# Performance work log

Hardware: AMD Instinct MI355X
Metric: run time of the kernel (lower is better)

The kernel has to match this reference:

```python
import jax, jax.numpy as jnp
import numpy as np
from jax import lax

DN = ('NCHW', 'OIHW', 'NCHW')

def _edge_bank():
    # All eight fixed stencils embedded in 5x5 (3x3 kernels zero-padded to center),
    # equivalent to the original per-kernel SAME conv. Order matches torch.cat order:
    # sobel_x, sobel_y, diag1, diag2, laplacian, gradient5x5, scharr_x, scharr_y
    k3 = [
        [[-1, 0, 1], [-2, 0, 2], [-1, 0, 1]],            # sobel_x
        [[-1, -2, -1], [0, 0, 0], [1, 2, 1]],            # sobel_y
        [[0, 1, 2], [-1, 0, 1], [-2, -1, 0]],            # diag1
        [[-2, -1, 0], [-1, 0, 1], [0, 1, 2]],            # diag2
        [[0, 1, 0], [1, -4, 1], [0, 1, 0]],              # laplacian
    ]
    g5 = [[-1, -2, 0, 2, 1], [-2, -3, 0, 3, 2], [-3, -4, 0, 4, 3],
          [-2, -3, 0, 3, 2], [-1, -2, 0, 2, 1]]          # gradient5x5
    s3 = [
        [[-3, 0, 3], [-10, 0, 10], [-3, 0, 3]],          # scharr_x
        [[-3, -10, -3], [0, 0, 0], [3, 10, 3]],          # scharr_y
    ]
    ks = []
    for k in k3:
        ks.append(np.pad(np.asarray(k, np.float32), 1))
    ks.append(np.asarray(g5, np.float32))
    for k in s3:
        ks.append(np.pad(np.asarray(k, np.float32), 1))
    return jnp.asarray(np.stack(ks)[:, None, :, :])  # [8,1,5,5]

EDGE_BANK = _edge_bank()

def _conv(x, w, p):
    return lax.conv_general_dilated(x, w, (1, 1), [(p, p), (p, p)], dimension_numbers=DN)

def setup_inputs() -> dict:
    key = jax.random.key(0)
    k = jax.random.split(key, 7)
    x  = jax.random.normal(k[0], (8, 1, 512, 512), jnp.float32)
    w1 = jax.random.normal(k[1], (32, 9, 3, 3), jnp.float32) * 0.05
    b1 = jax.random.normal(k[2], (32,), jnp.float32) * 0.01
    w2 = jax.random.normal(k[3], (16, 32, 3, 3), jnp.float32) * 0.05
    b2 = jax.random.normal(k[4], (16,), jnp.float32) * 0.01
    wr = jax.random.normal(k[5], (16, 1, 1, 1), jnp.float32) * 0.05
    br = jax.random.normal(k[6], (16,), jnp.float32) * 0.01
    return {"x": x, "w1": w1, "b1": b1, "w2": w2, "b2": b2, "wr": wr, "br": br}

def reference(x, w1, b1, w2, b2, wr, br):
    grads = _conv(x, EDGE_BANK, 2)                         # [B,8,H,W] all stencils in one pass
    feats = jnp.concatenate([grads, x], axis=1)            # [B,9,H,W]
    h = jax.nn.relu(_conv(feats, w1, 1) + b1[None, :, None, None])
    fused = jax.nn.relu(_conv(h, w2, 1) + b2[None, :, None, None])
    residual = _conv(x, wr, 0) + br[None, :, None, None]
    return fused + residual
```

## Files before the change

### kernel.cpp

```cpp
#include <hip/hip_runtime.h>
#include <hip/hip_bf16.h>


typedef __attribute__((ext_vector_type(8))) short bf16x8;
typedef __attribute__((ext_vector_type(4))) float f32x4;

#define XS_S 28

#define WS_A2   5120
#define WS_SB   9728
#define WS_FLT  5120
#define WS_WEFF 12800
#define WS_BYTES 30720

__device__ const float EB[9][5][5] = {
 {{0,0,0,0,0},{0,-1,0,1,0},{0,-2,0,2,0},{0,-1,0,1,0},{0,0,0,0,0}},
 {{0,0,0,0,0},{0,-1,-2,-1,0},{0,0,0,0,0},{0,1,2,1,0},{0,0,0,0,0}},
 {{0,0,0,0,0},{0,0,1,2,0},{0,-1,0,1,0},{0,-2,-1,0,0},{0,0,0,0,0}},
 {{0,0,0,0,0},{0,-2,-1,0,0},{0,-1,0,1,0},{0,0,1,2,0},{0,0,0,0,0}},
 {{0,0,0,0,0},{0,0,1,0,0},{0,1,-4,1,0},{0,0,1,0,0},{0,0,0,0,0}},
 {{-1,-2,0,2,1},{-2,-3,0,3,2},{-3,-4,0,4,3},{-2,-3,0,3,2},{-1,-2,0,2,1}},
 {{0,0,0,0,0},{0,-3,0,3,0},{0,-10,0,10,0},{0,-3,0,3,0},{0,0,0,0,0}},
 {{0,0,0,0,0},{0,-3,-10,-3,0},{0,0,0,0,0},{0,3,10,3,0},{0,0,0,0,0}},
 {{0,0,0,0,0},{0,0,0,0,0},{0,0,1,0,0},{0,0,0,0,0},{0,0,0,0,0}},
};

__device__ __forceinline__ unsigned short f2bf(float f) {
    union { float f; unsigned u; } v; v.f = f;
    unsigned u = v.u + 0x7fffu + ((v.u >> 16) & 1u);
    return (unsigned short)(u >> 16);
}

__device__ __forceinline__ float weff_tap(const float* __restrict__ w1,
                                          int oc, int dy, int dx) {
    float s = 0.f;
    for (int ch = 0; ch < 9; ++ch)
        for (int ty = 0; ty < 3; ++ty)
            for (int tx = 0; tx < 3; ++tx) {
                int sy = dy - ty, sx = dx - tx;
                if (sy >= 0 && sy < 5 && sx >= 0 && sx < 5)
                    s += w1[(oc * 9 + ch) * 9 + ty * 3 + tx] * EB[ch][sy][sx];
            }
    return s;
}

__global__ __launch_bounds__(256) void setup_frags(
    const float* __restrict__ w1, const float* __restrict__ b1,
    const float* __restrict__ w2, const float* __restrict__ b2,
    const float* __restrict__ wr, const float* __restrict__ br,
    short* __restrict__ ws)
{
    __shared__ float w1s[2592];
    __shared__ float w2s[4608];
    __shared__ float ebs[225];
    const int tid = threadIdx.x;

    for (int i = tid; i < 2592; i += 256) w1s[i] = w1[i];
    for (int i = tid; i < 4608; i += 256) w2s[i] = w2[i];
    if (tid < 225) ebs[tid] = ((const float*)EB)[tid];
    __syncthreads();

    for (int idx = tid; idx < 5120; idx += 256) {
        int i = idx & 7, lane = (idx >> 3) & 63, rest = idx >> 9;
        int mt = rest / 5, ks = rest - 5 * mt;
        int n = lane & 15, lg = lane >> 4;
        int k = 32 * ks + 8 * lg + i;
        int g = k >> 4, ch = k & 15;
        float w = (g < 9 && ch < 9) ? w1s[(mt * 16 + n) * 81 + ch * 9 + g] : 0.f;
        ws[idx] = (short)f2bf(w);
    }
    for (int idx = tid; idx < 4608; idx += 256) {
        int i = idx & 7, lane = (idx >> 3) & 63, ks = idx >> 9;
        int n = lane & 15, lg = lane >> 4;
        int ic = 8 * lg + i;
        ws[WS_A2 + idx] = (short)f2bf(w2s[n * 288 + ic * 9 + ks]);
    }
    for (int idx = tid; idx < 512; idx += 256) {
        int i = idx & 7, lane = idx >> 3;
        int n = lane & 15, lg = lane >> 4;
        int k = 8 * lg + i;
        float v = (k < 25 && n < 9) ? ebs[n * 25 + k] : 0.f;
        ws[WS_SB + idx] = (short)f2bf(v);
    }
    for (int idx = tid; idx < 2048; idx += 256) {
        int i = idx & 7, lane = (idx >> 3) & 63, rest = idx >> 9;
        int mt = rest >> 1, ks = rest & 1;
        int n = lane & 15, lg = lane >> 4;
        int dy = 4 * ks + lg, dx = i;
        float s = 0.f;
        if (dy < 7 && dx < 7) {
            int oc = mt * 16 + n;
            for (int ch = 0; ch < 9; ++ch)
                for (int ty = 0; ty < 3; ++ty) {
                    int sy = dy - ty;
                    if (sy < 0 || sy >= 5) continue;
                    for (int tx = 0; tx < 3; ++tx) {
                        int sx = dx - tx;
                        if (sx >= 0 && sx < 5)
                            s += w1s[(oc * 9 + ch) * 9 + ty * 3 + tx] * ebs[ch * 25 + sy * 5 + sx];
                    }
                }
        }
        ws[WS_WEFF + idx] = (short)f2bf(s);
    }
    if (tid < 64) {
        int lg = tid >> 4;
        float* wf = (float*)ws + WS_FLT + tid * 20;
        for (int r = 0; r < 4; ++r) {
            wf[r]      = b1[lg * 4 + r];
            wf[4 + r]  = b1[16 + lg * 4 + r];
            wf[8 + r]  = b2[lg * 4 + r];
            wf[12 + r] = wr[lg * 4 + r];
            wf[16 + r] = br[lg * 4 + r];
        }
    }
}

template<bool USE_WS>
__global__ __launch_bounds__(256, 3) void edge_interior2(
    const float* __restrict__ x,  const float* __restrict__ w1, const float* __restrict__ b1,
    const float* __restrict__ w2, const float* __restrict__ b2,
    const float* __restrict__ wr, const float* __restrict__ br,
    const short* __restrict__ ws, float* __restrict__ out)
{
    __shared__ long long pool[39936 / 8];
    __shared__ short xs[24 * 40 + 8];
    short* hs    = (short*)pool;
    float* stage = (float*)pool;

    const int tid  = threadIdx.x;
    const int lane = tid & 63;
    const int wave = tid >> 6;
    const int n    = lane & 15;
    const int lg   = lane >> 4;
    const int bx = blockIdx.x * 32, by = blockIdx.y * 16, b = blockIdx.z;

    for (int i = tid; i < 480; i += 256) {
        int r = i / 20, c2 = i % 20;
        int gy = by - 4 + r;  gy = gy < 0 ? 0 : (gy > 511 ? 511 : gy);
        int gx = bx - 4 + 2 * c2; gx = gx < 0 ? 0 : (gx > 510 ? 510 : gx);
        const float2 v = *reinterpret_cast<const float2*>(&x[((size_t)b * 512 + gy) * 512 + gx]);
        __hip_bfloat162 p0 = __float22bfloat162_rn(make_float2(v.x, v.y));
        *reinterpret_cast<unsigned*>(&xs[r * 40 + 2 * c2]) = *reinterpret_cast<unsigned*>(&p0);
    }

    bf16x8 wa[2][2], a2[9];
    float b1v[2][4], b2v[4], wrv[4], brv[4];
    if (USE_WS) {
#pragma unroll
        for (int mt = 0; mt < 2; ++mt)
#pragma unroll
            for (int ks = 0; ks < 2; ++ks)
                wa[mt][ks] = *reinterpret_cast<const bf16x8*>(
                    &ws[WS_WEFF + ((mt * 2 + ks) * 64 + lane) * 8]);
#pragma unroll
        for (int ks = 0; ks < 9; ++ks)
            a2[ks] = *reinterpret_cast<const bf16x8*>(&ws[WS_A2 + (ks * 64 + lane) * 8]);
        const float* wf = (const float*)ws + WS_FLT + lane * 20;
        f32x4 t0 = *reinterpret_cast<const f32x4*>(wf);
        f32x4 t1 = *reinterpret_cast<const f32x4*>(wf + 4);
        f32x4 t2 = *reinterpret_cast<const f32x4*>(wf + 8);
        f32x4 t3 = *reinterpret_cast<const f32x4*>(wf + 12);
        f32x4 t4 = *reinterpret_cast<const f32x4*>(wf + 16);
#pragma unroll
        for (int r = 0; r < 4; ++r) {
            b1v[0][r] = t0[r]; b1v[1][r] = t1[r];
            b2v[r] = t2[r]; wrv[r] = t3[r]; brv[r] = t4[r];
        }
    } else {
#pragma unroll
        for (int mt = 0; mt < 2; ++mt)
#pragma unroll
            for (int ks = 0; ks < 2; ++ks)
#pragma unroll
                for (int i = 0; i < 8; ++i) {
                    int dy = 4 * ks + lg, dx = i;
                    float s = (dy < 7 && dx < 7) ? weff_tap(w1, mt * 16 + n, dy, dx) : 0.f;
                    wa[mt][ks][i] = (short)f2bf(s);
                }
#pragma unroll
        for (int ks = 0; ks < 9; ++ks)
#pragma unroll
            for (int i = 0; i < 8; ++i)
                a2[ks][i] = (short)f2bf(w2[n * 288 + (8 * lg + i) * 9 + ks]);
#pragma unroll
        for (int r = 0; r < 4; ++r) {
            b1v[0][r] = b1[lg * 4 + r]; b1v[1][r] = b1[16 + lg * 4 + r];
            b2v[r] = b2[lg * 4 + r]; wrv[r] = wr[lg * 4 + r]; brv[r] = br[lg * 4 + r];
        }
    }

    __syncthreads();

    for (int t = wave; t < 39; t += 4) {
        int p  = t * 16 + n;
        int pc = p < 611 ? p : 611;
        int r1 = pc / 34, c1 = pc - 34 * r1;
        int base = r1 * 40 + c1;
        f32x4 acc0 = {0.f,0.f,0.f,0.f}, acc1 = {0.f,0.f,0.f,0.f};
#pragma unroll
        for (int ks = 0; ks < 2; ++ks) {
            const int dy = 4 * ks + lg;
            bf16x8 bv = {0,0,0,0,0,0,0,0};
            if (dy < 7) {
                const short* rp = &xs[base + dy * 40];
#pragma unroll
                for (int i = 0; i < 8; ++i) bv[i] = rp[i];
            }
            acc0 = __builtin_amdgcn_mfma_f32_16x16x32_bf16(wa[0][ks], bv, acc0, 0, 0, 0);
            acc1 = __builtin_amdgcn_mfma_f32_16x16x32_bf16(wa[1][ks], bv, acc1, 0, 0, 0);
        }
        if (p < 612) {
            __hip_bfloat162 q0 = __float22bfloat162_rn(make_float2(
                fmaxf(acc0[0] + b1v[0][0], 0.f), fmaxf(acc0[1] + b1v[0][1], 0.f)));
            __hip_bfloat162 q1 = __float22bfloat162_rn(make_float2(
                fmaxf(acc0[2] + b1v[0][2], 0.f), fmaxf(acc0[3] + b1v[0][3], 0.f)));
            uint2 W0; W0.x = *reinterpret_cast<unsigned*>(&q0);
            W0.y = *reinterpret_cast<unsigned*>(&q1);
            *reinterpret_cast<uint2*>(&hs[(((lg >> 1)) * 624 + p) * 8 + 4 * (lg & 1)]) = W0;
            __hip_bfloat162 q2 = __float22bfloat162_rn(make_float2(
                fmaxf(acc1[0] + b1v[1][0], 0.f), fmaxf(acc1[1] + b1v[1][1], 0.f)));
            __hip_bfloat162 q3 = __float22bfloat162_rn(make_float2(
                fmaxf(acc1[2] + b1v[1][2], 0.f), fmaxf(acc1[3] + b1v[1][3], 0.f)));
            uint2 W1; W1.x = *reinterpret_cast<unsigned*>(&q2);
            W1.y = *reinterpret_cast<unsigned*>(&q3);
            *reinterpret_cast<uint2*>(&hs[((2 + (lg >> 1)) * 624 + p) * 8 + 4 * (lg & 1)]) = W1;
        }
    }
    __syncthreads();

    const int hbase = lg * 624 * 8;
    f32x4 oreg[8];
#pragma unroll
    for (int j = 0; j < 8; ++j) {
        const int tj = wave + 4 * j;
        const int oy = tj >> 1, hh = tj & 1;
        f32x4 acc = {0.f,0.f,0.f,0.f};
#pragma unroll
        for (int ks = 0; ks < 9; ++ks) {
            const int dy = ks / 3, dx = ks - 3 * (ks / 3);
            const int px = (oy + dy) * 34 + 16 * hh + n + dx;
            bf16x8 hf = *reinterpret_cast<const bf16x8*>(&hs[hbase + px * 8]);
            acc = __builtin_amdgcn_mfma_f32_16x16x32_bf16(a2[ks], hf, acc, 0, 0, 0);
        }
        __hip_bfloat16 xh = *reinterpret_cast<const __hip_bfloat16*>(
            &xs[(oy + 4) * 40 + 16 * hh + n + 4]);
        float xv = __bfloat162float(xh);
        f32x4 o;
#pragma unroll
        for (int r = 0; r < 4; ++r)
            o[r] = fmaxf(acc[r] + b2v[r], 0.f) + wrv[r] * xv + brv[r];
        oreg[j] = o;
    }
    __syncthreads();

#pragma unroll
    for (int j = 0; j < 8; ++j) {
        const int tj = wave + 4 * j;
        const int oy = tj >> 1, hh = tj & 1;
#pragma unroll
        for (int r = 0; r < 4; ++r)
            stage[(lg * 4 + r) * 576 + oy * 36 + 16 * hh + n] = oreg[j][r];
    }
    __syncthreads();

#pragma unroll
    for (int k = 0; k < 8; ++k) {
        int idx = k * 256 + tid;
        int c   = idx & 7;
        int row = (idx >> 3) & 15;
        int oc  = idx >> 7;
        f32x4 v = *reinterpret_cast<const f32x4*>(&stage[oc * 576 + row * 36 + 4 * c]);
        __builtin_nontemporal_store(v, reinterpret_cast<f32x4*>(
            &out[(((size_t)b * 16 + oc) * 512 + (by + row)) * 512 + bx + 4 * c]));
    }
}

template<bool USE_WS>
__global__ __launch_bounds__(256, 4) void edge_border(
    const float* __restrict__ x,  const float* __restrict__ w1, const float* __restrict__ b1,
    const float* __restrict__ w2, const float* __restrict__ b2,
    const float* __restrict__ wr, const float* __restrict__ br,
    const short* __restrict__ ws, float* __restrict__ out)
{
    __shared__ short fs2[2 * 400 * 8];
    __shared__ short hs4[4 * 324 * 8];
    __shared__ short xs[24 * XS_S];

    const int tid  = threadIdx.x;
    const int lane = tid & 63;
    const int wave = tid >> 6;
    const int n    = lane & 15;
    const int lg   = lane >> 4;

    int idx = blockIdx.x, tx, ty;
    if      (idx < 32) { tx = idx;      ty = 0;  }
    else if (idx < 64) { tx = idx - 32; ty = 31; }
    else if (idx < 94) { tx = 0;        ty = idx - 63; }
    else               { tx = 31;       ty = idx - 93; }
    const int bx = tx * 16, by = ty * 16, b = blockIdx.z;

    for (int i = tid; i < 576; i += 256) {
        int r = i / 24, c = i % 24;
        int gy = by - 4 + r, gx = bx - 4 + c;
        float v = 0.f;
        if (gy >= 0 && gy < 512 && gx >= 0 && gx < 512) v = x[((size_t)b * 512 + gy) * 512 + gx];
        __hip_bfloat16 h = __float2bfloat16(v);
        xs[r * XS_S + c] = *reinterpret_cast<short*>(&h);
    }

    bf16x8 a1[2][5], a2[9], sb;
    float b1v[2][4], b2v[4], wrv[4], brv[4];
    if (USE_WS) {
#pragma unroll
        for (int mt = 0; mt < 2; ++mt)
#pragma unroll
            for (int ks = 0; ks < 5; ++ks)
                a1[mt][ks] = *reinterpret_cast<const bf16x8*>(&ws[((mt * 5 + ks) * 64 + lane) * 8]);
#pragma unroll
        for (int ks = 0; ks < 9; ++ks)
            a2[ks] = *reinterpret_cast<const bf16x8*>(&ws[WS_A2 + (ks * 64 + lane) * 8]);
        sb = *reinterpret_cast<const bf16x8*>(&ws[WS_SB + lane * 8]);
        const float* wf = (const float*)ws + WS_FLT + lane * 20;
        f32x4 t0 = *reinterpret_cast<const f32x4*>(wf);
        f32x4 t1 = *reinterpret_cast<const f32x4*>(wf + 4);
        f32x4 t2 = *reinterpret_cast<const f32x4*>(wf + 8);
        f32x4 t3 = *reinterpret_cast<const f32x4*>(wf + 12);
        f32x4 t4 = *reinterpret_cast<const f32x4*>(wf + 16);
#pragma unroll
        for (int r = 0; r < 4; ++r) {
            b1v[0][r] = t0[r]; b1v[1][r] = t1[r];
            b2v[r] = t2[r]; wrv[r] = t3[r]; brv[r] = t4[r];
        }
    } else {
#pragma unroll
        for (int mt = 0; mt < 2; ++mt)
#pragma unroll
            for (int ks = 0; ks < 5; ++ks)
#pragma unroll
                for (int i = 0; i < 8; ++i) {
                    int k = 32 * ks + 8 * lg + i;
                    int g = k >> 4, ch = k & 15;
                    float w = (g < 9 && ch < 9) ? w1[(mt * 16 + n) * 81 + ch * 9 + g] : 0.f;
                    a1[mt][ks][i] = (short)f2bf(w);
                }
#pragma unroll
        for (int ks = 0; ks < 9; ++ks)
#pragma unroll
            for (int i = 0; i < 8; ++i)
                a2[ks][i] = (short)f2bf(w2[n * 288 + (8 * lg + i) * 9 + ks]);
#pragma unroll
        for (int i = 0; i < 8; ++i) {
            int k = 8 * lg + i;
            float v = (k < 25 && n < 9) ? EB[n][k / 5][k % 5] : 0.f;
            sb[i] = (short)f2bf(v);
        }
#pragma unroll
        for (int r = 0; r < 4; ++r) {
            b1v[0][r] = b1[lg * 4 + r]; b1v[1][r] = b1[16 + lg * 4 + r];
            b2v[r] = b2[lg * 4 + r]; wrv[r] = wr[lg * 4 + r]; brv[r] = br[lg * 4 + r];
        }
    }

    int toff[8];
#pragma unroll
    for (int i = 0; i < 8; ++i) {
        int k = 8 * lg + i;
        int t = k < 25 ? k : 24;
        toff[i] = (t / 5) * XS_S + (t % 5);
    }
    int boff[5];
#pragma unroll
    for (int ks = 0; ks < 5; ++ks) {
        int g = 2 * ks + (lg >> 1); if (g > 8) g = 8;
        int dy = g / 3, dx = g - 3 * dy;
        boff[ks] = (lg & 1) * 3200 + (dy * 20 + dx) * 8;
    }

    __syncthreads();

    for (int t = wave; t < 25; t += 4) {
        int px = t * 16 + n;
        int r = px / 20, c = px - 20 * r;
        const short* base = &xs[r * XS_S + c];
        bf16x8 bv;
#pragma unroll
        for (int i = 0; i < 8; ++i) bv[i] = base[toff[i]];
        f32x4 f = {0.f, 0.f, 0.f, 0.f};
        f = __builtin_amdgcn_mfma_f32_16x16x32_bf16(sb, bv, f, 0, 0, 0);
        int fy = by + r - 2, fx = bx + c - 2;
        float m = (fy >= 0 && fy < 512 && fx >= 0 && fx < 512) ? 1.f : 0.f;
        __hip_bfloat162 p0 = __float22bfloat162_rn(make_float2(f[0] * m, f[1] * m));
        __hip_bfloat162 p1 = __float22bfloat162_rn(make_float2(f[2] * m, f[3] * m));
        uint2 wv;
        wv.x = *reinterpret_cast<unsigned*>(&p0);
        wv.y = *reinterpret_cast<unsigned*>(&p1);
        *reinterpret_cast<uint2*>(&fs2[((lg >> 1) * 400 + px) * 8 + 4 * (lg & 1)]) = wv;
    }
    __syncthreads();

    for (int t = wave; t < 21; t += 4) {
        int p  = t * 16 + n;
        int pc = p < 323 ? p : 323;
        int r1 = pc / 18, c1 = pc - 18 * r1;
        int base = (r1 * 20 + c1) * 8;
        f32x4 acc0 = {0.f,0.f,0.f,0.f}, acc1 = {0.f,0.f,0.f,0.f};
#pragma unroll
        for (int ks = 0; ks < 5; ++ks) {
            bf16x8 bf = *reinterpret_cast<const bf16x8*>(&fs2[base + boff[ks]]);
            acc0 = __builtin_amdgcn_mfma_f32_16x16x32_bf16(a1[0][ks], bf, acc0, 0, 0, 0);
            acc1 = __builtin_amdgcn_mfma_f32_16x16x32_bf16(a1[1][ks], bf, acc1, 0, 0, 0);
        }
        if (p < 324) {
            int hy = by - 1 + r1, hx = bx - 1 + c1;
            float m = (hy >= 0 && hy < 512 && hx >= 0 && hx < 512) ? 1.f : 0.f;
            __hip_bfloat162 q0 = __float22bfloat162_rn(make_float2(
                fmaxf(acc0[0] + b1v[0][0], 0.f) * m, fmaxf(acc0[1] + b1v[0][1], 0.f) * m));
            __hip_bfloat162 q1 = __float22bfloat162_rn(make_float2(
                fmaxf(acc0[2] + b1v[0][2], 0.f) * m, fmaxf(acc0[3] + b1v[0][3], 0.f) * m));
            uint2 W0; W0.x = *reinterpret_cast<unsigned*>(&q0);
            W0.y = *reinterpret_cast<unsigned*>(&q1);
            *reinterpret_cast<uint2*>(&hs4[((lg >> 1) * 324 + p) * 8 + 4 * (lg & 1)]) = W0;
            __hip_bfloat162 q2 = __float22bfloat162_rn(make_float2(
                fmaxf(acc1[0] + b1v[1][0], 0.f) * m, fmaxf(acc1[1] + b1v[1][1], 0.f) * m));
            __hip_bfloat162 q3 = __float22bfloat162_rn(make_float2(
                fmaxf(acc1[2] + b1v[1][2], 0.f) * m, fmaxf(acc1[3] + b1v[1][3], 0.f) * m));
            uint2 W1; W1.x = *reinterpret_cast<unsigned*>(&q2);
            W1.y = *reinterpret_cast<unsigned*>(&q3);
            *reinterpret_cast<uint2*>(&hs4[((2 + (lg >> 1)) * 324 + p) * 8 + 4 * (lg & 1)]) = W1;
        }
    }
    __syncthreads();

    const int hbase = lg * 324 * 8;
#pragma unroll
    for (int j = 0; j < 4; ++j) {
        int oy = wave + 4 * j;
        f32x4 acc = {0.f,0.f,0.f,0.f};
#pragma unroll
        for (int ks = 0; ks < 9; ++ks) {
            const int dy = ks / 3, dx = ks - 3 * (ks / 3);
            bf16x8 hf = *reinterpret_cast<const bf16x8*>(
                &hs4[hbase + ((oy + dy) * 18 + n + dx) * 8]);
            acc = __builtin_amdgcn_mfma_f32_16x16x32_bf16(a2[ks], hf, acc, 0, 0, 0);
        }
        __hip_bfloat16 xh = *reinterpret_cast<const __hip_bfloat16*>(&xs[(oy + 4) * XS_S + n + 4]);
        float xv = __bfloat162float(xh);
        float* op = out + (((size_t)(b * 16 + lg * 4) * 512 + (by + oy)) * 512) + bx + n;
#pragma unroll
        for (int r = 0; r < 4; ++r) {
            float o = fmaxf(acc[r] + b2v[r], 0.f) + wrv[r] * xv + brv[r];
            __builtin_nontemporal_store(o, op);
            op += 262144;
        }
    }
}

extern "C" void kernel_launch(void* const* d_in, const int* in_sizes, int n_in,
                              void* d_out, int out_size, void* d_ws, size_t ws_size,
                              hipStream_t stream) {
    const float* x  = (const float*)d_in[0];
    const float* w1 = (const float*)d_in[1];
    const float* b1 = (const float*)d_in[2];
    const float* w2 = (const float*)d_in[3];
    const float* b2 = (const float*)d_in[4];
    const float* wr = (const float*)d_in[5];
    const float* br = (const float*)d_in[6];
    float* out = (float*)d_out;
    short* ws = (short*)d_ws;

    dim3 block(256);
    dim3 gin(16, 32, 8);
    dim3 gbd(124, 1, 8);
    if (ws_size >= WS_BYTES) {
        hipLaunchKernelGGL(setup_frags, dim3(1), dim3(256), 0, stream,
                           w1, b1, w2, b2, wr, br, ws);
        hipLaunchKernelGGL(edge_interior2<true>, gin, block, 0, stream,
                           x, w1, b1, w2, b2, wr, br, ws, out);
        hipLaunchKernelGGL(edge_border<true>, gbd, block, 0, stream,
                           x, w1, b1, w2, b2, wr, br, ws, out);
    } else {
        hipLaunchKernelGGL(edge_interior2<false>, gin, block, 0, stream,
                           x, w1, b1, w2, b2, wr, br, ws, out);
        hipLaunchKernelGGL(edge_border<false>, gbd, block, 0, stream,
                           x, w1, b1, w2, b2, wr, br, ws, out);
    }
}
```

Before: 114.3 us.

## Restructure interior kernel: direct global x loads, interleaved swizzled h layout, row-reuse conv2

The interior kernel no longer stages x in shared memory. It reads x straight from global memory and converts it to bf16 in registers. The h tile is stored as interleaved 32-channel pixel rows with an XOR swizzle, and the w2 fragments are reordered to match that layout. Conv2 now loads each h row fragment once and reuses it across four output rows, which cuts LDS reads. The grid skips the top and bottom tile rows, occupancy is raised to 4 blocks, and border stores become plain stores. The trade-off is more redundant global loads and extra register pressure.

New measurement: 107.9 us. -5.6%, faster.

```diff
diff --git a/kernel.cpp b/kernel.cpp
--- a/kernel.cpp
+++ b/kernel.cpp
@@ -11,7 +11,8 @@
 #define WS_SB   9728
 #define WS_FLT  5120
 #define WS_WEFF 12800
-#define WS_BYTES 30720
+#define WS_A2I  14848
+#define WS_BYTES 38912
 
 __device__ const float EB[9][5][5] = {
  {{0,0,0,0,0},{0,-1,0,1,0},{0,-2,0,2,0},{0,-1,0,1,0},{0,0,0,0,0}},
@@ -30,6 +31,9 @@
     unsigned u = v.u + 0x7fffu + ((v.u >> 16) & 1u);
     return (unsigned short)(u >> 16);
 }
+__device__ __forceinline__ unsigned pk(float lo, float hi) {
+    return (unsigned)f2bf(lo) | ((unsigned)f2bf(hi) << 16);
+}
 
 __device__ __forceinline__ float weff_tap(const float* __restrict__ w1,
                                           int oc, int dy, int dx) {
@@ -74,6 +78,12 @@
         int n = lane & 15, lg = lane >> 4;
         int ic = 8 * lg + i;
         ws[WS_A2 + idx] = (short)f2bf(w2s[n * 288 + ic * 9 + ks]);
+    }
+    for (int idx = tid; idx < 4608; idx += 256) {
+        int i = idx & 7, lane = (idx >> 3) & 63, ks = idx >> 9;
+        int n = lane & 15, lg = lane >> 4;
+        int ic = ((i & 1) << 4) | (lg << 2) | ((i >> 1) & 3);
+        ws[WS_A2I + idx] = (short)f2bf(w2s[n * 288 + ic * 9 + ks]);
     }
     for (int idx = tid; idx < 512; idx += 256) {
         int i = idx & 7, lane = idx >> 3;
@@ -117,15 +127,14 @@
 }
 
 template<bool USE_WS>
-__global__ __launch_bounds__(256, 3) void edge_interior2(
+__global__ __launch_bounds__(256, 4) void edge_interior3(
     const float* __restrict__ x,  const float* __restrict__ w1, const float* __restrict__ b1,
     const float* __restrict__ w2, const float* __restrict__ b2,
     const float* __restrict__ wr, const float* __restrict__ br,
     const short* __restrict__ ws, float* __restrict__ out)
 {
-    __shared__ long long pool[39936 / 8];
-    __shared__ short xs[24 * 40 + 8];
-    short* hs    = (short*)pool;
+    __shared__ long long pool[39168 / 8];
+    short* hsS   = (short*)pool;
     float* stage = (float*)pool;
 
     const int tid  = threadIdx.x;
@@ -133,16 +142,10 @@
     const int wave = tid >> 6;
     const int n    = lane & 15;
     const int lg   = lane >> 4;
-    const int bx = blockIdx.x * 32, by = blockIdx.y * 16, b = blockIdx.z;
-
-    for (int i = tid; i < 480; i += 256) {
-        int r = i / 20, c2 = i % 20;
-        int gy = by - 4 + r;  gy = gy < 0 ? 0 : (gy > 511 ? 511 : gy);
-        int gx = bx - 4 + 2 * c2; gx = gx < 0 ? 0 : (gx > 510 ? 510 : gx);
-        const float2 v = *reinterpret_cast<const float2*>(&x[((size_t)b * 512 + gy) * 512 + gx]);
-        __hip_bfloat162 p0 = __float22bfloat162_rn(make_float2(v.x, v.y));
-        *reinterpret_cast<unsigned*>(&xs[r * 40 + 2 * c2]) = *reinterpret_cast<unsigned*>(&p0);
-    }
+    const int bx = blockIdx.x * 32;
+    const int by = (blockIdx.y + 1) * 16;
+    const int b  = blockIdx.z;
+    const float* xb = x + ((size_t)b << 18);
 
     bf16x8 wa[2][2], a2[9];
     float b1v[2][4], b2v[4], wrv[4], brv[4];
@@ -155,7 +158,7 @@
                     &ws[WS_WEFF + ((mt * 2 + ks) * 64 + lane) * 8]);
 #pragma unroll
         for (int ks = 0; ks < 9; ++ks)
-            a2[ks] = *reinterpret_cast<const bf16x8*>(&ws[WS_A2 + (ks * 64 + lane) * 8]);
+            a2[ks] = *reinterpret_cast<const bf16x8*>(&ws[WS_A2I + (ks * 64 + lane) * 8]);
         const float* wf = (const float*)ws + WS_FLT + lane * 20;
         f32x4 t0 = *reinterpret_cast<const f32x4*>(wf);
         f32x4 t1 = *reinterpret_cast<const f32x4*>(wf + 4);
@@ -181,86 +184,97 @@
 #pragma unroll
         for (int ks = 0; ks < 9; ++ks)
 #pragma unroll
-            for (int i = 0; i < 8; ++i)
-                a2[ks][i] = (short)f2bf(w2[n * 288 + (8 * lg + i) * 9 + ks]);
+            for (int i = 0; i < 8; ++i) {
+                int ic = ((i & 1) << 4) | (lg << 2) | ((i >> 1) & 3);
+                a2[ks][i] = (short)f2bf(w2[(n * 32 + ic) * 9 + ks]);
+            }
 #pragma unroll
         for (int r = 0; r < 4; ++r) {
             b1v[0][r] = b1[lg * 4 + r]; b1v[1][r] = b1[16 + lg * 4 + r];
             b2v[r] = b2[lg * 4 + r]; wrv[r] = wr[lg * 4 + r]; brv[r] = br[lg * 4 + r];
         }
     }
-
-    __syncthreads();
 
     for (int t = wave; t < 39; t += 4) {
         int p  = t * 16 + n;
         int pc = p < 611 ? p : 611;
         int r1 = pc / 34, c1 = pc - 34 * r1;
-        int base = r1 * 40 + c1;
+        int gxb = bx - 4 + c1; gxb = gxb < 0 ? 0 : (gxb > 504 ? 504 : gxb);
+        int gyb = by - 4 + r1;
         f32x4 acc0 = {0.f,0.f,0.f,0.f}, acc1 = {0.f,0.f,0.f,0.f};
 #pragma unroll
         for (int ks = 0; ks < 2; ++ks) {
             const int dy = 4 * ks + lg;
             bf16x8 bv = {0,0,0,0,0,0,0,0};
             if (dy < 7) {
-                const short* rp = &xs[base + dy * 40];
-#pragma unroll
-                for (int i = 0; i < 8; ++i) bv[i] = rp[i];
+                int gy = gyb + dy; gy = gy < 0 ? 0 : (gy > 511 ? 511 : gy);
+                const float* xp = xb + ((size_t)gy << 9) + gxb;
+                uint4 u;
+                u.x = pk(xp[0], xp[1]); u.y = pk(xp[2], xp[3]);
+                u.z = pk(xp[4], xp[5]); u.w = pk(xp[6], xp[7]);
+                bv = *reinterpret_cast<bf16x8*>(&u);
             }
             acc0 = __builtin_amdgcn_mfma_f32_16x16x32_bf16(wa[0][ks], bv, acc0, 0, 0, 0);
             acc1 = __builtin_amdgcn_mfma_f32_16x16x32_bf16(wa[1][ks], bv, acc1, 0, 0, 0);
         }
         if (p < 612) {
-            __hip_bfloat162 q0 = __float22bfloat162_rn(make_float2(
-                fmaxf(acc0[0] + b1v[0][0], 0.f), fmaxf(acc0[1] + b1v[0][1], 0.f)));
-            __hip_bfloat162 q1 = __float22bfloat162_rn(make_float2(
-                fmaxf(acc0[2] + b1v[0][2], 0.f), fmaxf(acc0[3] + b1v[0][3], 0.f)));
-            uint2 W0; W0.x = *reinterpret_cast<unsigned*>(&q0);
-            W0.y = *reinterpret_cast<unsigned*>(&q1);
-            *reinterpret_cast<uint2*>(&hs[(((lg >> 1)) * 624 + p) * 8 + 4 * (lg & 1)]) = W0;
-            __hip_bfloat162 q2 = __float22bfloat162_rn(make_float2(
-                fmaxf(acc1[0] + b1v[1][0], 0.f), fmaxf(acc1[1] + b1v[1][1], 0.f)));
-            __hip_bfloat162 q3 = __float22bfloat162_rn(make_float2(
-                fmaxf(acc1[2] + b1v[1][2], 0.f), fmaxf(acc1[3] + b1v[1][3], 0.f)));
-            uint2 W1; W1.x = *reinterpret_cast<unsigned*>(&q2);
-            W1.y = *reinterpret_cast<unsigned*>(&q3);
-            *reinterpret_cast<uint2*>(&hs[((2 + (lg >> 1)) * 624 + p) * 8 + 4 * (lg & 1)]) = W1;
-        }
-    }
-    __syncthreads();
-
-    const int hbase = lg * 624 * 8;
+            float h0 = fmaxf(acc0[0] + b1v[0][0], 0.f), g0 = fmaxf(acc1[0] + b1v[1][0], 0.f);
+            float h1 = fmaxf(acc0[1] + b1v[0][1], 0.f), g1 = fmaxf(acc1[1] + b1v[1][1], 0.f);
+            float h2 = fmaxf(acc0[2] + b1v[0][2], 0.f), g2 = fmaxf(acc1[2] + b1v[1][2], 0.f);
+            float h3 = fmaxf(acc0[3] + b1v[0][3], 0.f), g3 = fmaxf(acc1[3] + b1v[1][3], 0.f);
+            uint4 W;
+            W.x = pk(h0, g0); W.y = pk(h1, g1); W.z = pk(h2, g2); W.w = pk(h3, g3);
+            int grp = lg ^ (p & 3);
+            *reinterpret_cast<uint4*>(&hsS[p * 32 + grp * 8]) = W;
+        }
+    }
+    __syncthreads();
+
+    const int q0 = wave >> 1;
+    const int hh = wave & 1;
     f32x4 oreg[8];
 #pragma unroll
-    for (int j = 0; j < 8; ++j) {
-        const int tj = wave + 4 * j;
-        const int oy = tj >> 1, hh = tj & 1;
-        f32x4 acc = {0.f,0.f,0.f,0.f};
-#pragma unroll
-        for (int ks = 0; ks < 9; ++ks) {
-            const int dy = ks / 3, dx = ks - 3 * (ks / 3);
-            const int px = (oy + dy) * 34 + 16 * hh + n + dx;
-            bf16x8 hf = *reinterpret_cast<const bf16x8*>(&hs[hbase + px * 8]);
-            acc = __builtin_amdgcn_mfma_f32_16x16x32_bf16(a2[ks], hf, acc, 0, 0, 0);
-        }
-        __hip_bfloat16 xh = *reinterpret_cast<const __hip_bfloat16*>(
-            &xs[(oy + 4) * 40 + 16 * hh + n + 4]);
-        float xv = __bfloat162float(xh);
-        f32x4 o;
-#pragma unroll
-        for (int r = 0; r < 4; ++r)
-            o[r] = fmaxf(acc[r] + b2v[r], 0.f) + wrv[r] * xv + brv[r];
-        oreg[j] = o;
-    }
-    __syncthreads();
-
-#pragma unroll
-    for (int j = 0; j < 8; ++j) {
-        const int tj = wave + 4 * j;
-        const int oy = tj >> 1, hh = tj & 1;
-#pragma unroll
-        for (int r = 0; r < 4; ++r)
-            stage[(lg * 4 + r) * 576 + oy * 36 + 16 * hh + n] = oreg[j][r];
+    for (int j = 0; j < 2; ++j) {
+        const int q = q0 + 2 * j;
+        f32x4 acc[4] = {{0.f,0.f,0.f,0.f},{0.f,0.f,0.f,0.f},
+                        {0.f,0.f,0.f,0.f},{0.f,0.f,0.f,0.f}};
+#pragma unroll
+        for (int rr = 0; rr < 6; ++rr) {
+#pragma unroll
+            for (int dx = 0; dx < 3; ++dx) {
+                const int px = (4 * q + rr) * 34 + 16 * hh + n + dx;
+                const int grp = lg ^ (px & 3);
+                bf16x8 hf = *reinterpret_cast<const bf16x8*>(&hsS[px * 32 + grp * 8]);
+#pragma unroll
+                for (int o = 0; o < 4; ++o) {
+                    const int dy = rr - o;
+                    if (dy >= 0 && dy < 3)
+                        acc[o] = __builtin_amdgcn_mfma_f32_16x16x32_bf16(
+                            a2[dy * 3 + dx], hf, acc[o], 0, 0, 0);
+                }
+            }
+        }
+#pragma unroll
+        for (int o = 0; o < 4; ++o) {
+            const int oy = 4 * q + o;
+            float xv = xb[((size_t)(by + oy) << 9) + bx + 16 * hh + n];
+            f32x4 ov;
+#pragma unroll
+            for (int r = 0; r < 4; ++r)
+                ov[r] = fmaxf(acc[o][r] + b2v[r], 0.f) + wrv[r] * xv + brv[r];
+            oreg[4 * j + o] = ov;
+        }
+    }
+    __syncthreads();
+
+#pragma unroll
+    for (int j = 0; j < 2; ++j) {
+        const int q = q0 + 2 * j;
+#pragma unroll
+        for (int o = 0; o < 4; ++o)
+#pragma unroll
+            for (int r = 0; r < 4; ++r)
+                stage[(lg * 4 + r) * 576 + (4 * q + o) * 36 + 16 * hh + n] = oreg[4 * j + o][r];
     }
     __syncthreads();
 
@@ -390,11 +404,9 @@
         f = __builtin_amdgcn_mfma_f32_16x16x32_bf16(sb, bv, f, 0, 0, 0);
         int fy = by + r - 2, fx = bx + c - 2;
         float m = (fy >= 0 && fy < 512 && fx >= 0 && fx < 512) ? 1.f : 0.f;
-        __hip_bfloat162 p0 = __float22bfloat162_rn(make_float2(f[0] * m, f[1] * m));
-        __hip_bfloat162 p1 = __float22bfloat162_rn(make_float2(f[2] * m, f[3] * m));
         uint2 wv;
-        wv.x = *reinterpret_cast<unsigned*>(&p0);
-        wv.y = *reinterpret_cast<unsigned*>(&p1);
+        wv.x = pk(f[0] * m, f[1] * m);
+        wv.y = pk(f[2] * m, f[3] * m);
         *reinterpret_cast<uint2*>(&fs2[((lg >> 1) * 400 + px) * 8 + 4 * (lg & 1)]) = wv;
     }
     __syncthreads();
@@ -414,19 +426,13 @@
         if (p < 324) {
             int hy = by - 1 + r1, hx = bx - 1 + c1;
             float m = (hy >= 0 && hy < 512 && hx >= 0 && hx < 512) ? 1.f : 0.f;
-            __hip_bfloat162 q0 = __float22bfloat162_rn(make_float2(
-                fmaxf(acc0[0] + b1v[0][0], 0.f) * m, fmaxf(acc0[1] + b1v[0][1], 0.f) * m));
-            __hip_bfloat162 q1 = __float22bfloat162_rn(make_float2(
-                fmaxf(acc0[2] + b1v[0][2], 0.f) * m, fmaxf(acc0[3] + b1v[0][3], 0.f) * m));
-            uint2 W0; W0.x = *reinterpret_cast<unsigned*>(&q0);
-            W0.y = *reinterpret_cast<unsigned*>(&q1);
+            uint2 W0;
+            W0.x = pk(fmaxf(acc0[0] + b1v[0][0], 0.f) * m, fmaxf(acc0[1] + b1v[0][1], 0.f) * m);
+            W0.y = pk(fmaxf(acc0[2] + b1v[0][2], 0.f) * m, fmaxf(acc0[3] + b1v[0][3], 0.f) * m);
             *reinterpret_cast<uint2*>(&hs4[((lg >> 1) * 324 + p) * 8 + 4 * (lg & 1)]) = W0;
-            __hip_bfloat162 q2 = __float22bfloat162_rn(make_float2(
-                fmaxf(acc1[0] + b1v[1][0], 0.f) * m, fmaxf(acc1[1] + b1v[1][1], 0.f) * m));
-            __hip_bfloat162 q3 = __float22bfloat162_rn(make_float2(
-                fmaxf(acc1[2] + b1v[1][2], 0.f) * m, fmaxf(acc1[3] + b1v[1][3], 0.f) * m));
-            uint2 W1; W1.x = *reinterpret_cast<unsigned*>(&q2);
-            W1.y = *reinterpret_cast<unsigned*>(&q3);
+            uint2 W1;
+            W1.x = pk(fmaxf(acc1[0] + b1v[1][0], 0.f) * m, fmaxf(acc1[1] + b1v[1][1], 0.f) * m);
+            W1.y = pk(fmaxf(acc1[2] + b1v[1][2], 0.f) * m, fmaxf(acc1[3] + b1v[1][3], 0.f) * m);
             *reinterpret_cast<uint2*>(&hs4[((2 + (lg >> 1)) * 324 + p) * 8 + 4 * (lg & 1)]) = W1;
         }
     }
@@ -450,7 +456,7 @@
 #pragma unroll
         for (int r = 0; r < 4; ++r) {
             float o = fmaxf(acc[r] + b2v[r], 0.f) + wrv[r] * xv + brv[r];
-            __builtin_nontemporal_store(o, op);
+            *op = o;
             op += 262144;
         }
     }
@@ -470,17 +476,17 @@
     short* ws = (short*)d_ws;
 
     dim3 block(256);
-    dim3 gin(16, 32, 8);
+    dim3 gin(16, 30, 8);
     dim3 gbd(124, 1, 8);
     if (ws_size >= WS_BYTES) {
         hipLaunchKernelGGL(setup_frags, dim3(1), dim3(256), 0, stream,
                            w1, b1, w2, b2, wr, br, ws);
-        hipLaunchKernelGGL(edge_interior2<true>, gin, block, 0, stream,
+        hipLaunchKernelGGL(edge_interior3<true>, gin, block, 0, stream,
                            x, w1, b1, w2, b2, wr, br, ws, out);
         hipLaunchKernelGGL(edge_border<true>, gbd, block, 0, stream,
                            x, w1, b1, w2, b2, wr, br, ws, out);
     } else {
-        hipLaunchKernelGGL(edge_interior2<false>, gin, block, 0, stream,
+        hipLaunchKernelGGL(edge_interior3<false>, gin, block, 0, stream,
                            x, w1, b1, w2, b2, wr, br, ws, out);
         hipLaunchKernelGGL(edge_border<false>, gbd, block, 0, stream,
                            x, w1, b1, w2, b2, wr, br, ws, out);
```
